# Kernel tuning notes

Hardware: AMD Instinct MI355X
Metric: run time of the kernel (lower is better)

The kernel has to match this reference:

```python
import jax, jax.numpy as jnp
import numpy as np

B, S, H = 64, 2048, 1024


def setup_inputs() -> dict:
    key = jax.random.key(0)
    k1, k2, k3, k4 = jax.random.split(key, 4)
    hidden = jax.random.normal(k1, (1, B, H), dtype=jnp.float32)
    encoder_output = jax.random.normal(k2, (B, S, H), dtype=jnp.float32)
    # nn.Linear(H, H): weight (out, in) = (H, H), bias (H,)
    scale = 1.0 / np.sqrt(H)
    W = jax.random.uniform(k3, (H, H), dtype=jnp.float32, minval=-scale, maxval=scale)
    b = jax.random.uniform(k4, (H,), dtype=jnp.float32, minval=-scale, maxval=scale)
    return {"hidden": hidden, "encoder_output": encoder_output, "W": W, "b": b}


def reference(hidden, encoder_output, W, b):
    # hidden: (1, B, H) -> (B, H); encoder_output: (B, S, H)
    h = jnp.squeeze(hidden, axis=0)
    # 'general' score: energy[b, s] = h[b] . (Linear(enc[b, s]))
    #   Linear: enc @ W.T + b  (torch nn.Linear convention)
    proj = jnp.einsum('bsh,kh->bsk', encoder_output, W) + b  # (B, S, H)
    energies = jnp.einsum('bh,bsh->bs', h, proj)             # (B, S)
    # original applies softmax over dim=0 (batch axis) -- kept faithful
    return jax.nn.softmax(energies, axis=0)
```

## Files before the change

kernel.cpp:

```cpp
#include <hip/hip_runtime.h>
#include <math.h>

#define Bdim 64
#define Sdim 2048
#define Hdim 1024

__global__ __launch_bounds__(256)
void proj_v_kernel(const float* __restrict__ hid, const float* __restrict__ W,
                   const float* __restrict__ bias, float* __restrict__ v,
                   float* __restrict__ c)
{
    __shared__ float sh[Hdim];
    __shared__ float red[4];
    const int b   = blockIdx.y;
    const int tid = threadIdx.x;

    for (int i = tid; i < Hdim; i += 256) sh[i] = hid[b * Hdim + i];
    __syncthreads();

    if (blockIdx.x == 4) {
        float acc = 0.f;
        for (int k = tid; k < Hdim; k += 256) acc += sh[k] * bias[k];
        for (int off = 32; off > 0; off >>= 1) acc += __shfl_down(acc, off, 64);
        if ((tid & 63) == 0) red[tid >> 6] = acc;
        __syncthreads();
        if (tid == 0) c[b] = red[0] + red[1] + red[2] + red[3];
        return;
    }

    const int h = blockIdx.x * 256 + tid;
    const float* Wp = W + h;
    float acc = 0.f;
    #pragma unroll 8
    for (int k = 0; k < Hdim; ++k)
        acc = fmaf(sh[k], Wp[(size_t)k * Hdim], acc);
    v[b * Hdim + h] = acc;
}

__global__ __launch_bounds__(256)
void energy_kernel(const float* __restrict__ enc, const float* __restrict__ v,
                   const float* __restrict__ c, float* __restrict__ out)
{
    const int b      = blockIdx.y;
    const int lane   = threadIdx.x & 63;
    const int wave   = threadIdx.x >> 6;
    const int s_base = blockIdx.x * 32 + wave * 8;

    const float4* vrow = (const float4*)(v + b * Hdim);
    const float4 v0 = vrow[lane];
    const float4 v1 = vrow[lane + 64];
    const float4 v2 = vrow[lane + 128];
    const float4 v3 = vrow[lane + 192];
    const float  cb = c[b];

    const float4* erow = (const float4*)(enc + ((size_t)b * Sdim + s_base) * Hdim);

    #pragma unroll 2
    for (int i = 0; i < 8; ++i) {
        const float4* ep = erow + (size_t)i * (Hdim / 4);
        const float4 a0 = ep[lane];
        const float4 a1 = ep[lane + 64];
        const float4 a2 = ep[lane + 128];
        const float4 a3 = ep[lane + 192];

        float acc = a0.x * v0.x + a0.y * v0.y + a0.z * v0.z + a0.w * v0.w;
        acc      += a1.x * v1.x + a1.y * v1.y + a1.z * v1.z + a1.w * v1.w;
        acc      += a2.x * v2.x + a2.y * v2.y + a2.z * v2.z + a2.w * v2.w;
        acc      += a3.x * v3.x + a3.y * v3.y + a3.z * v3.z + a3.w * v3.w;

        #pragma unroll
        for (int off = 1; off < 64; off <<= 1)
            acc += __shfl_xor(acc, off, 64);

        if (lane == 0) out[b * Sdim + s_base + i] = acc + cb;
    }
}

__global__ __launch_bounds__(64)
void softmax_kernel(float* __restrict__ out)
{
    const int s = blockIdx.x * 64 + threadIdx.x;
    float vals[Bdim];
    #pragma unroll
    for (int b = 0; b < Bdim; ++b) vals[b] = out[b * Sdim + s];
    float m = vals[0];
    #pragma unroll
    for (int b = 1; b < Bdim; ++b) m = fmaxf(m, vals[b]);
    float sum = 0.f;
    #pragma unroll
    for (int b = 0; b < Bdim; ++b) { vals[b] = __expf(vals[b] - m); sum += vals[b]; }
    const float inv = 1.f / sum;
    #pragma unroll
    for (int b = 0; b < Bdim; ++b) out[b * Sdim + s] = vals[b] * inv;
}

extern "C" void kernel_launch(void* const* d_in, const int* in_sizes, int n_in,
                              void* d_out, int out_size, void* d_ws, size_t ws_size,
                              hipStream_t stream)
{
    const float* hid  = (const float*)d_in[0];
    const float* enc  = (const float*)d_in[1];
    const float* W    = (const float*)d_in[2];
    const float* bias = (const float*)d_in[3];
    float* out = (float*)d_out;

    float* v = (float*)d_ws;
    float* c = v + Bdim * Hdim;

    proj_v_kernel<<<dim3(5, Bdim), 256, 0, stream>>>(hid, W, bias, v, c);
    energy_kernel<<<dim3(Sdim / 32, Bdim), 256, 0, stream>>>(enc, v, c, out);
    softmax_kernel<<<dim3(Sdim / 64), 64, 0, stream>>>(out);
}
```

Before: 748.8 us.

## Split-K vectorized projection, nontemporal encoder loads, wave-split batch softmax

```diff
diff --git a/kernel.cpp b/kernel.cpp
--- a/kernel.cpp
+++ b/kernel.cpp
@@ -5,36 +5,55 @@
 #define Sdim 2048
 #define Hdim 1024
 
+typedef float f4 __attribute__((ext_vector_type(4)));
+
 __global__ __launch_bounds__(256)
 void proj_v_kernel(const float* __restrict__ hid, const float* __restrict__ W,
                    const float* __restrict__ bias, float* __restrict__ v,
                    float* __restrict__ c)
 {
     __shared__ float sh[Hdim];
-    __shared__ float red[4];
-    const int b   = blockIdx.y;
-    const int tid = threadIdx.x;
+    __shared__ f4    red[4][64];
+    __shared__ float cr[4];
 
-    for (int i = tid; i < Hdim; i += 256) sh[i] = hid[b * Hdim + i];
+    const int b    = blockIdx.y;
+    const int t    = threadIdx.x;
+    const int w    = t >> 6;
+    const int lane = t & 63;
+
+    for (int i = t; i < Hdim; i += 256) sh[i] = hid[b * Hdim + i];
     __syncthreads();
 
-    if (blockIdx.x == 4) {
-        float acc = 0.f;
-        for (int k = tid; k < Hdim; k += 256) acc += sh[k] * bias[k];
-        for (int off = 32; off > 0; off >>= 1) acc += __shfl_down(acc, off, 64);
-        if ((tid & 63) == 0) red[tid >> 6] = acc;
-        __syncthreads();
-        if (tid == 0) c[b] = red[0] + red[1] + red[2] + red[3];
-        return;
+    const f4* W4 = (const f4*)W;
+    const int j4 = blockIdx.x * 64 + lane;
+
+    f4 a0 = {0.f, 0.f, 0.f, 0.f};
+    f4 a1 = {0.f, 0.f, 0.f, 0.f};
+    const int k0 = w * 256;
+    #pragma unroll 4
+    for (int k = k0; k < k0 + 256; k += 2) {
+        const f4 w0 = W4[(size_t)k * 256 + j4];
+        const f4 w1 = W4[(size_t)(k + 1) * 256 + j4];
+        a0 += sh[k] * w0;
+        a1 += sh[k + 1] * w1;
+    }
+    a0 += a1;
+    red[w][lane] = a0;
+    __syncthreads();
+
+    if (w == 0) {
+        const f4 r = red[0][lane] + red[1][lane] + red[2][lane] + red[3][lane];
+        ((f4*)v)[b * 256 + j4] = r;
     }
 
-    const int h = blockIdx.x * 256 + tid;
-    const float* Wp = W + h;
-    float acc = 0.f;
-    #pragma unroll 8
-    for (int k = 0; k < Hdim; ++k)
-        acc = fmaf(sh[k], Wp[(size_t)k * Hdim], acc);
-    v[b * Hdim + h] = acc;
+    if (blockIdx.x == 0) {
+        float pc = 0.f;
+        for (int k = t; k < Hdim; k += 256) pc = fmaf(sh[k], bias[k], pc);
+        for (int off = 32; off > 0; off >>= 1) pc += __shfl_down(pc, off, 64);
+        if (lane == 0) cr[w] = pc;
+        __syncthreads();
+        if (t == 0) c[b] = cr[0] + cr[1] + cr[2] + cr[3];
+    }
 }
 
 __global__ __launch_bounds__(256)
@@ -46,22 +65,22 @@
     const int wave   = threadIdx.x >> 6;
     const int s_base = blockIdx.x * 32 + wave * 8;
 
-    const float4* vrow = (const float4*)(v + b * Hdim);
-    const float4 v0 = vrow[lane];
-    const float4 v1 = vrow[lane + 64];
-    const float4 v2 = vrow[lane + 128];
-    const float4 v3 = vrow[lane + 192];
-    const float  cb = c[b];
+    const f4* vrow = (const f4*)(v + b * Hdim);
+    const f4 v0 = vrow[lane];
+    const f4 v1 = vrow[lane + 64];
+    const f4 v2 = vrow[lane + 128];
+    const f4 v3 = vrow[lane + 192];
+    const float cb = c[b];
 
-    const float4* erow = (const float4*)(enc + ((size_t)b * Sdim + s_base) * Hdim);
+    const f4* erow = (const f4*)(enc + ((size_t)b * Sdim + s_base) * Hdim);
 
     #pragma unroll 2
     for (int i = 0; i < 8; ++i) {
-        const float4* ep = erow + (size_t)i * (Hdim / 4);
-        const float4 a0 = ep[lane];
-        const float4 a1 = ep[lane + 64];
-        const float4 a2 = ep[lane + 128];
-        const float4 a3 = ep[lane + 192];
+        const f4* ep = erow + (size_t)i * (Hdim / 4);
+        const f4 a0 = __builtin_nontemporal_load(ep + lane);
+        const f4 a1 = __builtin_nontemporal_load(ep + lane + 64);
+        const f4 a2 = __builtin_nontemporal_load(ep + lane + 128);
+        const f4 a3 = __builtin_nontemporal_load(ep + lane + 192);
 
         float acc = a0.x * v0.x + a0.y * v0.y + a0.z * v0.z + a0.w * v0.w;
         acc      += a1.x * v1.x + a1.y * v1.y + a1.z * v1.z + a1.w * v1.w;
@@ -76,22 +95,38 @@
     }
 }
 
-__global__ __launch_bounds__(64)
+__global__ __launch_bounds__(256)
 void softmax_kernel(float* __restrict__ out)
 {
-    const int s = blockIdx.x * 64 + threadIdx.x;
-    float vals[Bdim];
+    __shared__ float smax[4][64];
+    __shared__ float ssum[4][64];
+    const int t    = threadIdx.x;
+    const int w    = t >> 6;
+    const int lane = t & 63;
+    const int s    = blockIdx.x * 64 + lane;
+
+    float vals[16];
+    float m = -1e30f;
     #pragma unroll
-    for (int b = 0; b < Bdim; ++b) vals[b] = out[b * Sdim + s];
-    float m = vals[0];
-    #pragma unroll
-    for (int b = 1; b < Bdim; ++b) m = fmaxf(m, vals[b]);
+    for (int i = 0; i < 16; ++i) {
+        vals[i] = out[(size_t)(w * 16 + i) * Sdim + s];
+        m = fmaxf(m, vals[i]);
+    }
+    smax[w][lane] = m;
+    __syncthreads();
+    m = fmaxf(fmaxf(smax[0][lane], smax[1][lane]),
+              fmaxf(smax[2][lane], smax[3][lane]));
+
     float sum = 0.f;
     #pragma unroll
-    for (int b = 0; b < Bdim; ++b) { vals[b] = __expf(vals[b] - m); sum += vals[b]; }
-    const float inv = 1.f / sum;
+    for (int i = 0; i < 16; ++i) { vals[i] = __expf(vals[i] - m); sum += vals[i]; }
+    ssum[w][lane] = sum;
+    __syncthreads();
+    const float inv = 1.f / (ssum[0][lane] + ssum[1][lane] +
+                             ssum[2][lane] + ssum[3][lane]);
     #pragma unroll
-    for (int b = 0; b < Bdim; ++b) out[b * Sdim + s] = vals[b] * inv;
+    for (int i = 0; i < 16; ++i)
+        out[(size_t)(w * 16 + i) * Sdim + s] = vals[i] * inv;
 }
 
 extern "C" void kernel_launch(void* const* d_in, const int* in_sizes, int n_in,
@@ -107,7 +142,7 @@
     float* v = (float*)d_ws;
     float* c = v + Bdim * Hdim;
 
-    proj_v_kernel<<<dim3(5, Bdim), 256, 0, stream>>>(hid, W, bias, v, c);
+    proj_v_kernel<<<dim3(4, Bdim), 256, 0, stream>>>(hid, W, bias, v, c);
     energy_kernel<<<dim3(Sdim / 32, Bdim), 256, 0, stream>>>(enc, v, c, out);
-    softmax_kernel<<<dim3(Sdim / 64), 64, 0, stream>>>(out);
+    softmax_kernel<<<dim3(Sdim / 64), 256, 0, stream>>>(out);
 }
```

Result: faster. 682.0 us (-8.9%).
